# Kernel tuning notes

Measured on AMD Instinct MI355X. Metric: run time of the kernel, lower is better.

## Reference

```python
import jax, jax.numpy as jnp
import numpy as np

EMBED_DIM = 512
NUM_HEADS = 16
TGT_LEN = 1024
BSZ = 4
HEAD_DIM = EMBED_DIM // NUM_HEADS


def setup_inputs() -> dict:
    key = jax.random.key(0)
    ks = jax.random.split(key, 12)
    E = EMBED_DIM
    s = 1.0 / np.sqrt(E)
    query = jax.random.normal(ks[0], (TGT_LEN, BSZ, E), dtype=jnp.float32)
    attn_bias = jax.random.normal(ks[1], (BSZ * NUM_HEADS, TGT_LEN, TGT_LEN), dtype=jnp.float32)
    key_padding_mask = jax.random.randint(ks[2], (BSZ, TGT_LEN), 0, 2) == 1
    q_w = jax.random.normal(ks[3], (E, E), dtype=jnp.float32) * s
    q_b = jax.random.normal(ks[4], (E,), dtype=jnp.float32) * 0.02
    k_w = jax.random.normal(ks[5], (E, E), dtype=jnp.float32) * s
    k_b = jax.random.normal(ks[6], (E,), dtype=jnp.float32) * 0.02
    v_w = jax.random.normal(ks[7], (E, E), dtype=jnp.float32) * s
    v_b = jax.random.normal(ks[8], (E,), dtype=jnp.float32) * 0.02
    out_w = jax.random.normal(ks[9], (E, E), dtype=jnp.float32) * s
    out_b = jax.random.normal(ks[10], (E,), dtype=jnp.float32) * 0.02
    return {
        "query": query, "attn_bias": attn_bias, "key_padding_mask": key_padding_mask,
        "q_w": q_w, "q_b": q_b, "k_w": k_w, "k_b": k_b,
        "v_w": v_w, "v_b": v_b, "out_w": out_w, "out_b": out_b,
    }


def reference(query, attn_bias, key_padding_mask, q_w, q_b, k_w, k_b, v_w, v_b, out_w, out_b):
    Tlen, B, E = query.shape
    H, hd = NUM_HEADS, HEAD_DIM
    scaling = hd ** -0.5
    # self-attention: q/k/v all from query (Linear uses y = x @ W.T + b)
    q = (query @ q_w.T + q_b) * scaling
    k = query @ k_w.T + k_b
    v = query @ v_w.T + v_b
    # [T, B, E] -> [B*H, T, hd]
    q = q.reshape(Tlen, B * H, hd).transpose(1, 0, 2)
    k = k.reshape(Tlen, B * H, hd).transpose(1, 0, 2)
    v = v.reshape(Tlen, B * H, hd).transpose(1, 0, 2)
    # scores [B*H, T, S]
    aw = jnp.einsum('bth,bsh->bts', q, k) + attn_bias
    # key padding mask: [B, S] -> broadcast over heads and tgt
    aw = aw.reshape(B, H, Tlen, Tlen)
    aw = jnp.where(key_padding_mask[:, None, None, :], -jnp.inf, aw)
    aw = aw.reshape(B * H, Tlen, Tlen)
    probs = jax.nn.softmax(aw.astype(jnp.float32), axis=-1)
    attn = jnp.einsum('bts,bsh->bth', probs.astype(query.dtype), v)
    attn = attn.transpose(1, 0, 2).reshape(Tlen, B, E)
    out = attn @ out_w.T + out_b
    # need_weights=True, need_head_weights=False -> mean over heads, [B, T, S]
    attn_weights_avg = probs.reshape(B, H, Tlen, Tlen).mean(axis=1)
    return out, attn_weights_avg
```

## Files before the change

kernel.cpp:

```cpp
#include <hip/hip_runtime.h>
#include <math.h>

typedef __bf16 bf16x8 __attribute__((ext_vector_type(8)));
typedef __bf16 bf16x4 __attribute__((ext_vector_type(4)));
typedef float  f32x4  __attribute__((ext_vector_type(4)));

__global__ __launch_bounds__(256)
void cvt_w(const float* __restrict__ w0, const float* __restrict__ w1,
           const float* __restrict__ w2, const float* __restrict__ w3,
           __bf16* __restrict__ d0, __bf16* __restrict__ d1,
           __bf16* __restrict__ d2, __bf16* __restrict__ d3)
{
    const int y = blockIdx.y;
    const float* s = (y == 0) ? w0 : (y == 1) ? w1 : (y == 2) ? w2 : w3;
    __bf16*      d = (y == 0) ? d0 : (y == 1) ? d1 : (y == 2) ? d2 : d3;
    const int i = blockIdx.x * 256 + threadIdx.x;
    float4 a = *(const float4*)(s + (size_t)i * 8);
    float4 b = *(const float4*)(s + (size_t)i * 8 + 4);
    bf16x8 v;
    v[0] = (__bf16)a.x; v[1] = (__bf16)a.y; v[2] = (__bf16)a.z; v[3] = (__bf16)a.w;
    v[4] = (__bf16)b.x; v[5] = (__bf16)b.y; v[6] = (__bf16)b.z; v[7] = (__bf16)b.w;
    *(bf16x8*)(d + (size_t)i * 8) = v;
}

__global__ __launch_bounds__(256, 2)
void qkv_proj(const float* __restrict__ X,
              const __bf16* __restrict__ Wqb, const __bf16* __restrict__ Wkb,
              const __bf16* __restrict__ Wvb,
              const float* __restrict__ bq, const float* __restrict__ bk,
              const float* __restrict__ bv,
              __bf16* __restrict__ qTb, __bf16* __restrict__ kTb,
              __bf16* __restrict__ vTb)
{
    const int tid  = threadIdx.x;
    const int w    = tid >> 6;
    const int lane = tid & 63;
    const int lq   = lane & 15;
    const int quad = lane >> 4;
    const int n0    = blockIdx.x * 64 + (w >> 1) * 32;
    const int obase = blockIdx.y * 128 + (w & 1) * 64;

    const __bf16* const Wz[3] = { Wqb, Wkb, Wvb };

    f32x4 acc[3][2][4] = {};
    for (int k0 = 0; k0 < 512; k0 += 32) {
        bf16x8 af[2];
#pragma unroll
        for (int m = 0; m < 2; m++) {
            const float* xp = X + (size_t)(n0 + m * 16 + lq) * 512 + k0 + quad * 8;
            float4 x0 = *(const float4*)xp;
            float4 x1 = *(const float4*)(xp + 4);
            bf16x8 v;
            v[0] = (__bf16)x0.x; v[1] = (__bf16)x0.y; v[2] = (__bf16)x0.z; v[3] = (__bf16)x0.w;
            v[4] = (__bf16)x1.x; v[5] = (__bf16)x1.y; v[6] = (__bf16)x1.z; v[7] = (__bf16)x1.w;
            af[m] = v;
        }
#pragma unroll
        for (int z = 0; z < 3; z++) {
            bf16x8 bfr[4];
#pragma unroll
            for (int nn = 0; nn < 4; nn++)
                bfr[nn] = *(const bf16x8*)(Wz[z] + (size_t)(obase + nn * 16 + lq) * 512 + k0 + quad * 8);
#pragma unroll
            for (int m = 0; m < 2; m++)
#pragma unroll
                for (int nn = 0; nn < 4; nn++)
                    acc[z][m][nn] = __builtin_amdgcn_mfma_f32_16x16x32_bf16(af[m], bfr[nn], acc[z][m][nn], 0, 0, 0);
        }
    }

    const float* const ba[3] = { bq, bk, bv };
    const float scaling = 0.17677669529663687f;
#pragma unroll
    for (int z = 0; z < 3; z++)
#pragma unroll
        for (int m = 0; m < 2; m++)
#pragma unroll
            for (int nn = 0; nn < 4; nn++)
#pragma unroll
                for (int r = 0; r < 4; r++) {
                    const int n = n0 + m * 16 + quad * 4 + r;
                    const int o = obase + nn * 16 + lq;
                    float val = acc[z][m][nn][r] + ba[z][o];
                    const int t = n >> 2, b = n & 3;
                    const int h = o >> 5, d = o & 31;
                    const int bh = b * 16 + h;
                    if (z == 0)
                        qTb[(((size_t)bh * 1024 + t) << 5) + d] = (__bf16)(val * scaling);
                    else if (z == 1)
                        kTb[(((size_t)bh * 1024 + t) << 5) + d] = (__bf16)val;
                    else
                        vTb[(((size_t)bh * 32 + d) << 10) + t] = (__bf16)val;
                }
}

__global__ __launch_bounds__(256)
void out_proj(const __bf16* __restrict__ A, const __bf16* __restrict__ Wb,
              const float* __restrict__ bias, float* __restrict__ out)
{
    const int tid  = threadIdx.x;
    const int w    = tid >> 6;
    const int lane = tid & 63;
    const int lq   = lane & 15;
    const int quad = lane >> 4;
    const int n0    = blockIdx.x * 64 + (w >> 1) * 32;
    const int obase = blockIdx.y * 128 + (w & 1) * 64;

    f32x4 acc[2][4] = {};
    for (int k0 = 0; k0 < 512; k0 += 32) {
        bf16x8 af[2], bfr[4];
#pragma unroll
        for (int m = 0; m < 2; m++)
            af[m] = *(const bf16x8*)(A + (size_t)(n0 + m * 16 + lq) * 512 + k0 + quad * 8);
#pragma unroll
        for (int nn = 0; nn < 4; nn++)
            bfr[nn] = *(const bf16x8*)(Wb + (size_t)(obase + nn * 16 + lq) * 512 + k0 + quad * 8);
#pragma unroll
        for (int m = 0; m < 2; m++)
#pragma unroll
            for (int nn = 0; nn < 4; nn++)
                acc[m][nn] = __builtin_amdgcn_mfma_f32_16x16x32_bf16(af[m], bfr[nn], acc[m][nn], 0, 0, 0);
    }
#pragma unroll
    for (int m = 0; m < 2; m++)
#pragma unroll
        for (int nn = 0; nn < 4; nn++)
#pragma unroll
            for (int r = 0; r < 4; r++) {
                const int n = n0 + m * 16 + quad * 4 + r;
                const int o = obase + nn * 16 + lq;
                out[(size_t)n * 512 + o] = acc[m][nn][r] + bias[o];
            }
}

__global__ __attribute__((amdgpu_waves_per_eu(2, 2))) __launch_bounds__(512)
void attn_mfma(const __bf16* __restrict__ qTb, const __bf16* __restrict__ kTb,
               const __bf16* __restrict__ vTb, const float* __restrict__ bias,
               const int* __restrict__ mask, __bf16* __restrict__ attnb,
               float* __restrict__ avgf, __bf16* __restrict__ p1)
{
    __shared__ float smem[20800];
    float* const Op0  = smem;
    float* const red0 = &smem[8448];
    __bf16* const Pbase = (__bf16*)&smem[8704];

    const int tid  = threadIdx.x;
    const int w    = tid >> 6;
    const int lane = tid & 63;
    const int lq   = lane & 15;
    const int quad = lane >> 4;

    const int bid = blockIdx.z * 128 + blockIdx.y * 32 + blockIdx.x;
    const int swz = (bid & 7) * 32 + (bid >> 3);
    const int t0  = (swz & 31) * 32;
    const int b   = (swz >> 5) & 3;
    const int z   = swz >> 7;
    const int sbase = w * 128;

    __bf16* const Pw = Pbase + w * 2176;

    unsigned mbits = 0;
    {
        const int* mp = mask + b * 1024 + sbase + quad * 4;
#pragma unroll
        for (int j = 0; j < 8; j++) {
            int4 m4 = *(const int4*)(mp + j * 16);
            mbits |= (unsigned)(m4.x != 0) << (j * 4 + 0);
            mbits |= (unsigned)(m4.y != 0) << (j * 4 + 1);
            mbits |= (unsigned)(m4.z != 0) << (j * 4 + 2);
            mbits |= (unsigned)(m4.w != 0) << (j * 4 + 3);
        }
    }

    const float* const bb = bias + (((size_t)(b * 16 + z * 8)) << 20) +
                            (((size_t)(t0 + lq)) << 10) + sbase + quad * 4;
    const __bf16* const qp0 = qTb + (((size_t)((b * 16 + z * 8) * 1024 + t0)) << 5) +
                              lq * 32 + quad * 8;
    const __bf16* const kp0 = kTb + ((size_t)(b * 16 + z * 8) << 15);
    const __bf16* const vp0 = vTb + ((size_t)(b * 16 + z * 8) << 15);

    bf16x8 qa = *(const bf16x8*)qp0;
    f32x4 cj[8];
#pragma unroll
    for (int j = 0; j < 8; j++) cj[j] = *(const f32x4*)(bb + j * 16);

    float avg0[32] = {}, avg1[32] = {};
    bf16x8 kb[8];
    bf16x8 v0r[4], v1r[4];

    auto body = [&](int hh, int ts, float (&avg)[32]) {
        float* const Op  = Op0  + ts * 4224;
        float* const red = red0 + ts * 128;

        if (ts == 0) {
            const __bf16* kp = kp0 + ((size_t)hh << 15);
            const __bf16* vp = vp0 + ((size_t)hh << 15);
#pragma unroll
            for (int j = 0; j < 8; j++)
                kb[j] = *(const bf16x8*)(kp + (size_t)(sbase + j * 16 + lq) * 32 + quad * 8);
#pragma unroll
            for (int ks = 0; ks < 4; ks++) {
                v0r[ks] = *(const bf16x8*)(vp + (size_t)lq * 1024 + sbase + ks * 32 + quad * 8);
                v1r[ks] = *(const bf16x8*)(vp + (size_t)(16 + lq) * 1024 + sbase + ks * 32 + quad * 8);
            }
        }
        __builtin_amdgcn_sched_barrier(0);

        f32x4 acc[8];
#pragma unroll
        for (int j = 0; j < 8; j++)
            acc[j] = __builtin_amdgcn_mfma_f32_16x16x32_bf16(kb[j], qa, cj[j], 0, 0, 0);
        __builtin_amdgcn_sched_barrier(0);

        {
            const int hn  = (ts == 0) ? hh : ((hh + 1) & 7);
            const int tsn = ts ^ 1;
            qa = *(const bf16x8*)(qp0 + ((size_t)hn << 15) + (tsn << 9));
            const float* bn = bb + ((size_t)hn << 20) + (tsn << 14);
#pragma unroll
            for (int j = 0; j < 8; j++) cj[j] = *(const f32x4*)(bn + j * 16);
        }
        __builtin_amdgcn_sched_barrier(0);

        float sm = 0.f;
#pragma unroll
        for (int j = 0; j < 8; j++)
#pragma unroll
            for (int r = 0; r < 4; r++) {
                float p = __expf(acc[j][r]);
                p = ((mbits >> (j * 4 + r)) & 1u) ? 0.f : p;
                acc[j][r] = p;
                sm += p;
            }
        sm += __shfl_xor(sm, 16);
        sm += __shfl_xor(sm, 32);

#pragma unroll
        for (int j = 0; j < 8; j++) {
            bf16x4 pv;
            pv[0] = (__bf16)acc[j][0]; pv[1] = (__bf16)acc[j][1];
            pv[2] = (__bf16)acc[j][2]; pv[3] = (__bf16)acc[j][3];
            *(bf16x4*)&Pw[lq * 136 + j * 16 + quad * 4] = pv;
        }
        if (lane < 16) red[w * 16 + lane] = sm;

        f32x4 o0 = {0.f, 0.f, 0.f, 0.f}, o1 = {0.f, 0.f, 0.f, 0.f};
#pragma unroll
        for (int ks = 0; ks < 4; ks++) {
            bf16x8 pa = *(const bf16x8*)&Pw[lq * 136 + ks * 32 + quad * 8];
            o0 = __builtin_amdgcn_mfma_f32_16x16x32_bf16(pa, v0r[ks], o0, 0, 0, 0);
            o1 = __builtin_amdgcn_mfma_f32_16x16x32_bf16(pa, v1r[ks], o1, 0, 0, 0);
        }
#pragma unroll
        for (int r = 0; r < 4; r++) {
            Op[w * 528 + (quad * 4 + r) * 33 + lq]      = o0[r];
            Op[w * 528 + (quad * 4 + r) * 33 + 16 + lq] = o1[r];
        }

        __builtin_amdgcn_sched_barrier(0);
        asm volatile("s_waitcnt lgkmcnt(0)" ::: "memory");
        __builtin_amdgcn_s_barrier();
        __builtin_amdgcn_sched_barrier(0);

        {
            const int t = tid >> 5, d = tid & 31;
            float s = 0.f, o = 0.f;
#pragma unroll
            for (int w2 = 0; w2 < 8; w2++) s += red[w2 * 16 + t];
#pragma unroll
            for (int w2 = 0; w2 < 8; w2++) o += Op[w2 * 528 + t * 33 + d];
            attnb[((size_t)(t0 + ts * 16 + t) * 4 + b) * 512 + (z * 8 + hh) * 32 + d] =
                (__bf16)(o / s);
        }

        float s_all = 0.f;
#pragma unroll
        for (int w2 = 0; w2 < 8; w2++) s_all += red[w2 * 16 + lq];
        const float inv = 1.0f / s_all;
#pragma unroll
        for (int j = 0; j < 8; j++)
#pragma unroll
            for (int r = 0; r < 4; r++)
                avg[j * 4 + r] += acc[j][r] * inv;
    };

    for (int hh = 0; hh < 8; hh++) {
        body(hh, 0, avg0);
        body(hh, 1, avg1);
    }

#pragma unroll
    for (int ts = 0; ts < 2; ts++) {
        const float* avg = ts ? avg1 : avg0;
        const size_t rowbase = ((size_t)(b * 1024 + t0 + ts * 16 + lq) << 10) +
                               sbase + quad * 4;
        if (z == 0) {
            float* ap = avgf + rowbase;
#pragma unroll
            for (int j = 0; j < 8; j++) {
                f32x4 v = { avg[j * 4 + 0] * 0.0625f, avg[j * 4 + 1] * 0.0625f,
                            avg[j * 4 + 2] * 0.0625f, avg[j * 4 + 3] * 0.0625f };
                *(f32x4*)(ap + j * 16) = v;
            }
        } else {
            __bf16* pp = p1 + rowbase;
#pragma unroll
            for (int j = 0; j < 8; j++) {
                bf16x4 v;
                v[0] = (__bf16)(avg[j * 4 + 0] * 0.0625f);
                v[1] = (__bf16)(avg[j * 4 + 1] * 0.0625f);
                v[2] = (__bf16)(avg[j * 4 + 2] * 0.0625f);
                v[3] = (__bf16)(avg[j * 4 + 3] * 0.0625f);
                *(bf16x4*)(pp + j * 16) = v;
            }
        }
    }
}

__global__ __launch_bounds__(256)
void avg_add(float* __restrict__ avg, const __bf16* __restrict__ p1)
{
    const size_t i = ((size_t)blockIdx.x * 256 + threadIdx.x) * 8;
    bf16x8 a = *(const bf16x8*)(p1 + i);
    float4 lo = *(float4*)(avg + i);
    float4 hi = *(float4*)(avg + i + 4);
    lo.x += (float)a[0]; lo.y += (float)a[1];
    lo.z += (float)a[2]; lo.w += (float)a[3];
    hi.x += (float)a[4]; hi.y += (float)a[5];
    hi.z += (float)a[6]; hi.w += (float)a[7];
    *(float4*)(avg + i)     = lo;
    *(float4*)(avg + i + 4) = hi;
}

extern "C" void kernel_launch(void* const* d_in, const int* in_sizes, int n_in,
                              void* d_out, int out_size, void* d_ws, size_t ws_size,
                              hipStream_t stream)
{
    const float* query     = (const float*)d_in[0];
    const float* attn_bias = (const float*)d_in[1];
    const int*   mask      = (const int*)d_in[2];
    const float* q_w       = (const float*)d_in[3];
    const float* q_b       = (const float*)d_in[4];
    const float* k_w       = (const float*)d_in[5];
    const float* k_b       = (const float*)d_in[6];
    const float* v_w       = (const float*)d_in[7];
    const float* v_b       = (const float*)d_in[8];
    const float* out_w     = (const float*)d_in[9];
    const float* out_b     = (const float*)d_in[10];

    float* out     = (float*)d_out;
    float* avg_out = out + (size_t)2097152;

    char* wsb = (char*)d_ws;
    __bf16* Wqb   = (__bf16*)(wsb);
    __bf16* Wkb   = (__bf16*)(wsb + ((size_t)512 << 10));
    __bf16* Wvb   = (__bf16*)(wsb + ((size_t)1 << 20));
    __bf16* Wob   = (__bf16*)(wsb + ((size_t)1 << 20) + ((size_t)512 << 10));
    __bf16* qTb   = (__bf16*)(wsb + ((size_t)2  << 20));
    __bf16* kTb   = (__bf16*)(wsb + ((size_t)6  << 20));
    __bf16* vTb   = (__bf16*)(wsb + ((size_t)10 << 20));
    __bf16* attnb = (__bf16*)(wsb + ((size_t)14 << 20));
    __bf16* p1    = (__bf16*)(wsb + ((size_t)18 << 20));

    cvt_w<<<dim3(128, 4), dim3(256), 0, stream>>>(
        q_w, k_w, v_w, out_w, Wqb, Wkb, Wvb, Wob);

    qkv_proj<<<dim3(64, 4), dim3(256), 0, stream>>>(
        query, Wqb, Wkb, Wvb, q_b, k_b, v_b, qTb, kTb, vTb);

    attn_mfma<<<dim3(32, 4, 2), dim3(512), 0, stream>>>(
        qTb, kTb, vTb, attn_bias, mask, attnb, avg_out, p1);

    avg_add<<<dim3(2048), dim3(256), 0, stream>>>(avg_out, p1);

    out_proj<<<dim3(64, 4), dim3(256), 0, stream>>>(attnb, Wob, out_b, out);
}
```

Measured before the change: 145.1 us.

## Prefetch attention bias tiles into LDS via direct global-to-LDS loads

Replaces the per-lane register prefetch of the fp32 attention-bias tile with buffer loads that write straight into a per-wave, XOR-swizzled LDS slot. The bias is read back from LDS with explicit vmcnt/lgkmcnt waits, and the next tile's load is issued before the score MFMAs. The waves_per_eu(2,2) attribute is dropped. Together these aim to free registers and let the largest global stream overlap compute. In exchange, shared memory grows substantially, which may cut occupancy, and correctness now rests on hand-written waitcnt counts.

Measured after the change: 213.2 us. 1.47x slower.

```diff
diff --git a/kernel.cpp b/kernel.cpp
--- a/kernel.cpp
+++ b/kernel.cpp
@@ -4,6 +4,13 @@
 typedef __bf16 bf16x8 __attribute__((ext_vector_type(8)));
 typedef __bf16 bf16x4 __attribute__((ext_vector_type(4)));
 typedef float  f32x4  __attribute__((ext_vector_type(4)));
+
+__device__ __forceinline__ void gload16(const float* g, float* l)
+{
+    __builtin_amdgcn_global_load_lds(
+        (const __attribute__((address_space(1))) void*)g,
+        (__attribute__((address_space(3))) void*)l, 16, 0, 0);
+}
 
 __global__ __launch_bounds__(256)
 void cvt_w(const float* __restrict__ w0, const float* __restrict__ w1,
@@ -133,13 +140,13 @@
             }
 }
 
-__global__ __attribute__((amdgpu_waves_per_eu(2, 2))) __launch_bounds__(512)
+__global__ __launch_bounds__(512)
 void attn_mfma(const __bf16* __restrict__ qTb, const __bf16* __restrict__ kTb,
                const __bf16* __restrict__ vTb, const float* __restrict__ bias,
                const int* __restrict__ mask, __bf16* __restrict__ attnb,
                float* __restrict__ avgf, __bf16* __restrict__ p1)
 {
-    __shared__ float smem[20800];
+    __shared__ float smem[33792];
     float* const Op0  = smem;
     float* const red0 = &smem[8448];
     __bf16* const Pbase = (__bf16*)&smem[8704];
@@ -149,6 +156,8 @@
     const int lane = tid & 63;
     const int lq   = lane & 15;
     const int quad = lane >> 4;
+    const int srow = lane >> 5;
+    const int schk = lane & 31;
 
     const int bid = blockIdx.z * 128 + blockIdx.y * 32 + blockIdx.x;
     const int swz = (bid & 7) * 32 + (bid >> 3);
@@ -157,7 +166,8 @@
     const int z   = swz >> 7;
     const int sbase = w * 128;
 
-    __bf16* const Pw = Pbase + w * 2176;
+    __bf16* const Pw  = Pbase + w * 2176;
+    float*  const slotB = &smem[17408 + w * 2048];
 
     unsigned mbits = 0;
     {
@@ -172,25 +182,41 @@
         }
     }
 
-    const float* const bb = bias + (((size_t)(b * 16 + z * 8)) << 20) +
-                            (((size_t)(t0 + lq)) << 10) + sbase + quad * 4;
-    const __bf16* const qp0 = qTb + (((size_t)((b * 16 + z * 8) * 1024 + t0)) << 5) +
+    const float* const biasW = bias + (((size_t)(b * 16 + z * 8)) << 20) +
+                               (size_t)t0 * 1024 + sbase;
+    const __bf16* const qpW = qTb + (((size_t)((b * 16 + z * 8) * 1024 + t0)) << 5) +
                               lq * 32 + quad * 8;
     const __bf16* const kp0 = kTb + ((size_t)(b * 16 + z * 8) << 15);
     const __bf16* const vp0 = vTb + ((size_t)(b * 16 + z * 8) << 15);
 
-    bf16x8 qa = *(const bf16x8*)qp0;
-    f32x4 cj[8];
-#pragma unroll
-    for (int j = 0; j < 8; j++) cj[j] = *(const f32x4*)(bb + j * 16);
+#pragma unroll
+    for (int k = 0; k < 8; k++) {
+        const int row = 2 * k + srow;
+        const int c   = schk ^ (row & 7);
+        gload16(biasW + (size_t)row * 1024 + c * 4, slotB + k * 256);
+    }
+    bf16x8 qa = *(const bf16x8*)qpW;
 
     float avg0[32] = {}, avg1[32] = {};
     bf16x8 kb[8];
     bf16x8 v0r[4], v1r[4];
 
     auto body = [&](int hh, int ts, float (&avg)[32]) {
+        const int i  = hh * 2 + ts;
+        const int in = (i + 1) & 15;
         float* const Op  = Op0  + ts * 4224;
         float* const red = red0 + ts * 128;
+
+        __builtin_amdgcn_sched_barrier(0);
+        asm volatile("s_waitcnt vmcnt(1)" ::: "memory");
+        __builtin_amdgcn_sched_barrier(0);
+
+        f32x4 cj[8];
+#pragma unroll
+        for (int j = 0; j < 8; j++)
+            cj[j] = *(const f32x4*)&slotB[lq * 128 + (((j * 4 + quad) ^ (lq & 7)) << 2)];
+        asm volatile("s_waitcnt lgkmcnt(0)" ::: "memory");
+        __builtin_amdgcn_sched_barrier(0);
 
         if (ts == 0) {
             const __bf16* kp = kp0 + ((size_t)hh << 15);
@@ -206,20 +232,23 @@
         }
         __builtin_amdgcn_sched_barrier(0);
 
+        bf16x8 qc = qa;
+        {
+            const float* src = biasW + ((size_t)(in >> 1) << 20) + ((in & 1) << 14);
+#pragma unroll
+            for (int k = 0; k < 8; k++) {
+                const int row = 2 * k + srow;
+                const int c   = schk ^ (row & 7);
+                gload16(src + (size_t)row * 1024 + c * 4, slotB + k * 256);
+            }
+            qa = *(const bf16x8*)(qpW + ((size_t)(in >> 1) << 15) + ((in & 1) << 9));
+        }
+        __builtin_amdgcn_sched_barrier(0);
+
         f32x4 acc[8];
 #pragma unroll
         for (int j = 0; j < 8; j++)
-            acc[j] = __builtin_amdgcn_mfma_f32_16x16x32_bf16(kb[j], qa, cj[j], 0, 0, 0);
-        __builtin_amdgcn_sched_barrier(0);
-
-        {
-            const int hn  = (ts == 0) ? hh : ((hh + 1) & 7);
-            const int tsn = ts ^ 1;
-            qa = *(const bf16x8*)(qp0 + ((size_t)hn << 15) + (tsn << 9));
-            const float* bn = bb + ((size_t)hn << 20) + (tsn << 14);
-#pragma unroll
-            for (int j = 0; j < 8; j++) cj[j] = *(const f32x4*)(bn + j * 16);
-        }
+            acc[j] = __builtin_amdgcn_mfma_f32_16x16x32_bf16(kb[j], qc, cj[j], 0, 0, 0);
         __builtin_amdgcn_sched_barrier(0);
 
         float sm = 0.f;
```
